# Optimization experiments

Hardware: AMD Instinct MI355X
Metric: run time of the kernel (lower is better)

## Reference

```python
import jax, jax.numpy as jnp
import numpy as np

E = 8          # number of routed experts
TOP_K = 2      # experts per token
D = 2048       # hidden size
DFF = 1408     # per-expert intermediate
DFF_S = 2816   # shared-expert intermediate (2 shared experts fused)
B, S = 2, 2048


def setup_inputs() -> dict:
    key = jax.random.key(0)
    ks = jax.random.split(key, 8)
    sc = 0.02
    return {
        "hidden_states": jax.random.normal(ks[0], (B, S, D), jnp.float32),
        "gate_weight": jax.random.normal(ks[1], (E, D), jnp.float32) * sc,
        "w_gate": jax.random.normal(ks[2], (E, DFF, D), jnp.float32) * sc,
        "w_up": jax.random.normal(ks[3], (E, DFF, D), jnp.float32) * sc,
        "w_down": jax.random.normal(ks[4], (E, D, DFF), jnp.float32) * sc,
        "w_shared_gate": jax.random.normal(ks[5], (DFF_S, D), jnp.float32) * sc,
        "w_shared_up": jax.random.normal(ks[6], (DFF_S, D), jnp.float32) * sc,
        "w_shared_down": jax.random.normal(ks[7], (D, DFF_S), jnp.float32) * sc,
    }


def reference(hidden_states, gate_weight, w_gate, w_up, w_down,
              w_shared_gate, w_shared_up, w_shared_down):
    orig_shape = hidden_states.shape
    x = hidden_states.reshape(-1, orig_shape[-1])      # [T, D]

    # --- router (computed under no_grad in the original) ---
    logits = x @ gate_weight.T                          # [T, E]
    scores = jax.nn.softmax(logits, axis=-1)
    topk_w, topk_idx = jax.lax.top_k(scores, TOP_K)     # [T, K]
    topk_w = topk_w / jnp.sum(topk_w, axis=-1, keepdims=True)
    topk_w = jax.lax.stop_gradient(topk_w)
    topk_idx = jax.lax.stop_gradient(topk_idx)

    # dense combine weights [T, E] (equivalent to the masked per-expert loop +
    # weighted sum over the top-k copies)
    combine = jnp.einsum('tk,tke->te', topk_w,
                         jax.nn.one_hot(topk_idx, E, dtype=x.dtype))

    # --- routed experts: SwiGLU MLP per expert, dense over E ---
    g = jnp.einsum('td,efd->etf', x, w_gate)            # [E, T, DFF]
    u = jnp.einsum('td,efd->etf', x, w_up)
    h = jax.nn.silu(g) * u
    expert_out = jnp.einsum('etf,edf->etd', h, w_down)  # [E, T, D]
    y = jnp.einsum('etd,te->td', expert_out, combine)   # [T, D]

    # --- shared experts on the identity ---
    sh = jax.nn.silu(x @ w_shared_gate.T) * (x @ w_shared_up.T)
    y = y + sh @ w_shared_down.T

    return y.reshape(orig_shape)
```

## Files before the change

kernel.cpp:

```cpp
#include <hip/hip_runtime.h>
#include <stdint.h>
#include <stdio.h>

#define T_TOK 4096
#define DMODEL 2048
#define NEXP 8
#define DFF 1408
#define DFFS 2816
#define NSLOT 8192

#define GU_GRID (16 * 22 + 39 * 11)
#define DN_GRID (16 * 8 + 39 * 8)
#define CONV_GU 1024
#define CONV_DN 512

typedef unsigned short u16;
typedef short s16x8 __attribute__((ext_vector_type(8)));
typedef unsigned short u16x4 __attribute__((ext_vector_type(4)));
typedef __bf16 bf16x8 __attribute__((ext_vector_type(8)));
typedef float f32x4 __attribute__((ext_vector_type(4)));

__device__ __forceinline__ u16 f2bf(float f) {
  uint32_t u = __builtin_bit_cast(uint32_t, f);
  u += 0x7fffu + ((u >> 16) & 1u);
  return (u16)(u >> 16);
}
__device__ __forceinline__ float bf2f(u16 h) {
  uint32_t u = ((uint32_t)h) << 16;
  return __builtin_bit_cast(float, u);
}

__device__ __forceinline__ void gl16(const u16* g, u16* l) {
  __builtin_amdgcn_global_load_lds((const __attribute__((address_space(1))) void*)g,
                                   (__attribute__((address_space(3))) void*)l,
                                   16, 0, 0);
}

#define BARRIER() asm volatile("s_barrier" ::: "memory")
#define SBAR()    __builtin_amdgcn_sched_barrier(0)

__device__ __forceinline__ void conv8(const float* __restrict__ s, u16* __restrict__ d,
                                      long k) {
  float4 a = ((const float4*)s)[2 * k];
  float4 b = ((const float4*)s)[2 * k + 1];
  s16x8 r;
  r[0] = (short)f2bf(a.x); r[1] = (short)f2bf(a.y);
  r[2] = (short)f2bf(a.z); r[3] = (short)f2bf(a.w);
  r[4] = (short)f2bf(b.x); r[5] = (short)f2bf(b.y);
  r[6] = (short)f2bf(b.z); r[7] = (short)f2bf(b.w);
  ((s16x8*)d)[k] = r;
}

__global__ void k_zero(int* __restrict__ counts) {
  if (threadIdx.x < NEXP) counts[threadIdx.x] = 0;
}

__global__ void k_router(const float* __restrict__ x, const float* __restrict__ gw,
                         u16* __restrict__ xb,
                         float* __restrict__ tkw, int* __restrict__ tki,
                         int* __restrict__ counts,
                         const float* __restrict__ wgF, u16* __restrict__ wbg,
                         const float* __restrict__ wuF, u16* __restrict__ wbu,
                         const float* __restrict__ wsgF, u16* __restrict__ wbsg,
                         const float* __restrict__ wsuF, u16* __restrict__ wbsu) {
  if (blockIdx.x >= T_TOK) {
    const long N1 = (long)NEXP * DFF * DMODEL / 8;
    const long NS = (long)DFFS * DMODEL / 8;
    const long total = 2 * N1 + 2 * NS;
    const long stride = (long)CONV_GU * 256;
    for (long i = (long)(blockIdx.x - T_TOK) * 256 + threadIdx.x; i < total; i += stride) {
      long k = i;
      if (k < N1)            conv8(wgF, wbg, k);
      else { k -= N1;
        if (k < N1)          conv8(wuF, wbu, k);
        else { k -= N1;
          if (k < NS)        conv8(wsgF, wbsg, k);
          else               conv8(wsuF, wbsu, k - NS);
        }
      }
    }
    return;
  }
  __shared__ double sm[NEXP];
  int t = blockIdx.x;
  int tid = threadIdx.x;
  int lane = tid & 63, wv = tid >> 6;
  const float4* xr = (const float4*)(x + (size_t)t * DMODEL);
  const float4* gr = (const float4*)gw;
  int e0 = wv * 2, e1 = e0 + 1;
  double a0 = 0.0, a1 = 0.0;
#pragma unroll
  for (int it = 0; it < DMODEL / 4 / 64; ++it) {
    int idx = it * 64 + lane;
    float4 xv = xr[idx];
    float4 g0 = gr[e0 * (DMODEL / 4) + idx];
    float4 g1 = gr[e1 * (DMODEL / 4) + idx];
    a0 += (double)xv.x * g0.x + (double)xv.y * g0.y +
          (double)xv.z * g0.z + (double)xv.w * g0.w;
    a1 += (double)xv.x * g1.x + (double)xv.y * g1.y +
          (double)xv.z * g1.z + (double)xv.w * g1.w;
    if (wv == 0) {
      u16x4 r = { f2bf(xv.x), f2bf(xv.y), f2bf(xv.z), f2bf(xv.w) };
      ((u16x4*)(xb + (size_t)t * DMODEL))[idx] = r;
    }
  }
#pragma unroll
  for (int off = 32; off; off >>= 1) {
    a0 += __shfl_down(a0, off, 64);
    a1 += __shfl_down(a1, off, 64);
  }
  if (lane == 0) { sm[e0] = a0; sm[e1] = a1; }
  __syncthreads();
  if (tid == 0) {
    double acc[NEXP];
#pragma unroll
    for (int e = 0; e < NEXP; ++e) acc[e] = sm[e];
    int i0 = 0; double v0 = acc[0];
    for (int e = 1; e < NEXP; ++e) if (acc[e] > v0) { v0 = acc[e]; i0 = e; }
    int i1 = -1; double v1 = -1e300;
    for (int e = 0; e < NEXP; ++e) if (e != i0 && acc[e] > v1) { v1 = acc[e]; i1 = e; }
    double r = exp(v1 - v0);
    float w0 = (float)(1.0 / (1.0 + r));
    float w1 = 1.0f - w0;
    tkw[2 * t] = w0; tkw[2 * t + 1] = w1;
    tki[2 * t] = i0; tki[2 * t + 1] = i1;
    atomicAdd(&counts[i0], 1);
    atomicAdd(&counts[i1], 1);
  }
}

__global__ void k_scan_sched(const int* __restrict__ counts, int* __restrict__ offs,
                             int* __restrict__ cursor, int* __restrict__ tblGU,
                             int* __restrict__ tblDN, int* __restrict__ nact) {
  if (threadIdx.x != 0 || blockIdx.x != 0) return;
  int s = 0;
  for (int e = 0; e < NEXP; ++e) { offs[e] = s; cursor[e] = s; s += counts[e]; }
  offs[NEXP] = s;
  int g = 0, d = 0;
  for (int m = 0; m < T_TOK / 256; ++m) {
    for (int nb = 0; nb < DFFS / 128; ++nb)
      tblGU[g++] = (int)(0x80000000u | (m << 12) | nb);
    for (int nb = 0; nb < DMODEL / 256; ++nb)
      tblDN[d++] = (int)(0x80000000u | (m << 12) | nb);
  }
  for (int e = 0; e < NEXP; ++e) {
    int mb = (counts[e] + 255) >> 8;
    for (int m = 0; m < mb; ++m) {
      for (int nb = 0; nb < DFF / 128; ++nb)
        tblGU[g++] = (e << 24) | (m << 12) | nb;
      for (int nb = 0; nb < DMODEL / 256; ++nb)
        tblDN[d++] = (e << 24) | (m << 12) | nb;
    }
  }
  nact[0] = g; nact[1] = d;
}

__global__ void k_assign(const int* __restrict__ tki, int* __restrict__ cursor,
                         int* __restrict__ pos, int* __restrict__ slot_tok) {
  int t = blockIdx.x * 256 + threadIdx.x;
  if (t >= T_TOK) return;
#pragma unroll
  for (int k = 0; k < 2; ++k) {
    int e = tki[2 * t + k];
    int p = atomicAdd(&cursor[e], 1);
    pos[2 * t + k] = p;
    slot_tok[p] = t;
  }
}

template <int PHASE>
__launch_bounds__(512, 2)
__global__ void k_gemm8(const int* __restrict__ tbl, const int* __restrict__ nact,
                        const u16* __restrict__ xb,
                        const u16* __restrict__ hr, const u16* __restrict__ hs,
                        const u16* __restrict__ wbg, const u16* __restrict__ wbu,
                        const u16* __restrict__ wbd,
                        const u16* __restrict__ wbsg, const u16* __restrict__ wbsu,
                        const u16* __restrict__ wbsd,
                        const float* __restrict__ wdF, const float* __restrict__ wsdF,
                        u16* __restrict__ wbdW, u16* __restrict__ wbsdW,
                        u16* __restrict__ P1r, u16* __restrict__ P1s,
                        u16* __restrict__ yr, float* __restrict__ out,
                        const int* __restrict__ offs, const int* __restrict__ counts,
                        const int* __restrict__ slot_tok) {
  __shared__ __attribute__((aligned(16))) u16 lds[2 * 32768];

  if constexpr (PHASE == 0) {
    if ((int)blockIdx.x >= GU_GRID) {
      const long N1 = (long)NEXP * DMODEL * DFF / 8;
      const long NS = (long)DMODEL * DFFS / 8;
      const long total = N1 + NS;
      const long stride = (long)CONV_DN * 512;
      for (long i = (long)(blockIdx.x - GU_GRID) * 512 + threadIdx.x; i < total;
           i += stride) {
        if (i < N1) conv8(wdF, wbdW, i);
        else        conv8(wsdF, wbsdW, i - N1);
      }
      return;
    }
  }
  if ((int)blockIdx.x >= nact[PHASE]) return;
  const int desc = tbl[blockIdx.x];
  const bool shrd = desc < 0;
  const int e = (desc >> 24) & 0xF;
  const int m0 = ((desc >> 12) & 0xFFF) * 256;
  const int n0 = (desc & 0xFFF) * (PHASE == 0 ? 128 : 256);

  const u16 *A, *Bg, *Bu;
  u16* C1;
  float* OF = nullptr;
  int base, cnt, HS, K;
  bool gather = false;
  if constexpr (PHASE == 0) {
    K = DMODEL;
    if (shrd) {
      A = xb; base = 0; cnt = T_TOK;
      Bg = wbsg; Bu = wbsu; C1 = P1s; HS = DFFS;
    } else {
      A = xb; gather = true; base = offs[e]; cnt = counts[e];
      size_t es = (size_t)e * DFF * DMODEL;
      Bg = wbg + es; Bu = wbu + es; C1 = P1r; HS = DFF;
    }
  } else {
    HS = DMODEL;
    if (shrd) {
      A = hs; base = 0; cnt = T_TOK; K = DFFS;
      Bg = Bu = wbsd; OF = out; C1 = nullptr;
    } else {
      A = hr; base = offs[e]; cnt = counts[e]; K = DFF;
      Bg = Bu = wbd + (size_t)e * DMODEL * DFF; C1 = yr;
    }
  }
  const int NT = K >> 6;

  int tid = threadIdx.x;
  int lane = tid & 63, wv = tid >> 6;
  int wm = wv >> 2, wn = wv & 3;
  int fr = lane & 15, fq = lane >> 4;

  int srow = tid >> 3;
  int sslot = (tid & 7) ^ (srow & 7);
  const u16* ap[4]; const u16* bp[4];
#pragma unroll
  for (int h = 0; h < 4; ++h) {
    int r = h * 64 + srow;
    int ra = m0 + r; ra = ra < cnt ? ra : cnt - 1;
    int ga = gather ? slot_tok[base + ra] : base + ra;
    ap[h] = A + (size_t)ga * K + sslot * 8;
    const u16* bb;
    if constexpr (PHASE == 0) {
      int wnr = r >> 6, s = r & 63;
      int col = n0 + wnr * 32 + (s & 31);
      bb = (s < 32 ? Bg : Bu) + (size_t)col * K;
    } else {
      bb = Bg + (size_t)(n0 + r) * K;
    }
    bp[h] = bb + sslot * 8;
  }

#define STG_A(h, bufi, kt) gl16(ap[h] + (size_t)(kt) * 64, \
                                lds + (bufi) * 32768 + (h) * 4096 + wv * 512)
#define STG_B(h, bufi, kt) gl16(bp[h] + (size_t)(kt) * 64, \
                                lds + (bufi) * 32768 + 16384 + (h) * 4096 + wv * 512)

  int sKs0 = ((0 + fq) ^ (fr & 7)) * 8;
  int sKs1 = ((4 + fq) ^ (fr & 7)) * 8;
  int aBase = wm * 8192 + fr * 64;
  int bBase = 16384 + (wn >> 1) * 8192 + ((wn & 1) * 64 + fr) * 64;

  f32x4 acc[8][4];
#pragma unroll
  for (int i = 0; i < 8; ++i)
#pragma unroll
    for (int j = 0; j < 4; ++j) acc[i][j] = (f32x4){0.f, 0.f, 0.f, 0.f};

  STG_A(0, 0, 0); STG_A(1, 0, 0); STG_A(2, 0, 0); STG_A(3, 0, 0);
  STG_B(0, 0, 0); STG_B(1, 0, 0); STG_B(2, 0, 0); STG_B(3, 0, 0);
  if (NT > 1) { STG_A(0, 1, 1); STG_A(1, 1, 1); STG_A(2, 1, 1); STG_A(3, 1, 1); }
  if (NT > 1) asm volatile("s_waitcnt vmcnt(4)" ::: "memory");
  else        asm volatile("s_waitcnt vmcnt(0)" ::: "memory");
  BARRIER();
  SBAR();

  bf16x8 rAa[4][2], rAb[4][2], rB01[2][2], rB23[2][2];
#pragma unroll
  for (int il = 0; il < 4; ++il) {
    rAa[il][0] = *(const bf16x8*)(lds + aBase + il * 1024 + sKs0);
    rAa[il][1] = *(const bf16x8*)(lds + aBase + il * 1024 + sKs1);
  }
#pragma unroll
  for (int jl = 0; jl < 2; ++jl) {
    rB01[jl][0] = *(const bf16x8*)(lds + bBase + jl * 1024 + sKs0);
    rB01[jl][1] = *(const bf16x8*)(lds + bBase + jl * 1024 + sKs1);
  }

  for (int t = 0; t < NT; ++t) {
    const int buf = t & 1, nbuf = buf ^ 1;
    const u16* lbuf = lds + buf * 32768;
    const u16* lbufN = lds + nbuf * 32768;
    const bool hn1 = (t + 1) < NT, hn2 = (t + 2) < NT;

#pragma unroll
    for (int jl = 0; jl < 2; ++jl) {
      rB23[jl][0] = *(const bf16x8*)(lbuf + bBase + (2 + jl) * 1024 + sKs0);
      rB23[jl][1] = *(const bf16x8*)(lbuf + bBase + (2 + jl) * 1024 + sKs1);
    }
    if (hn1) { STG_B(0, nbuf, t + 1); STG_B(1, nbuf, t + 1); }
    __builtin_amdgcn_s_setprio(1);
#pragma unroll
    for (int il = 0; il < 4; ++il)
#pragma unroll
      for (int jl = 0; jl < 2; ++jl) {
        acc[il][jl] = __builtin_amdgcn_mfma_f32_16x16x32_bf16(rAa[il][0], rB01[jl][0], acc[il][jl], 0, 0, 0);
        acc[il][jl] = __builtin_amdgcn_mfma_f32_16x16x32_bf16(rAa[il][1], rB01[jl][1], acc[il][jl], 0, 0, 0);
      }
    __builtin_amdgcn_s_setprio(0);

#pragma unroll
    for (int il = 0; il < 4; ++il) {
      rAb[il][0] = *(const bf16x8*)(lbuf + aBase + (4 + il) * 1024 + sKs0);
      rAb[il][1] = *(const bf16x8*)(lbuf + aBase + (4 + il) * 1024 + sKs1);
    }
    if (hn1) { STG_B(2, nbuf, t + 1); STG_B(3, nbuf, t + 1); }
    __builtin_amdgcn_s_setprio(1);
#pragma unroll
    for (int il = 0; il < 4; ++il)
#pragma unroll
      for (int jl = 0; jl < 2; ++jl) {
        acc[il][2 + jl] = __builtin_amdgcn_mfma_f32_16x16x32_bf16(rAa[il][0], rB23[jl][0], acc[il][2 + jl], 0, 0, 0);
        acc[il][2 + jl] = __builtin_amdgcn_mfma_f32_16x16x32_bf16(rAa[il][1], rB23[jl][1], acc[il][2 + jl], 0, 0, 0);
      }
    __builtin_amdgcn_s_setprio(0);

    asm volatile("s_waitcnt lgkmcnt(0)" ::: "memory");
    BARRIER();
    SBAR();
    if (hn2) { STG_A(0, buf, t + 2); STG_A(1, buf, t + 2); }
    __builtin_amdgcn_s_setprio(1);
#pragma unroll
    for (int il = 0; il < 4; ++il)
#pragma unroll
      for (int jl = 0; jl < 2; ++jl) {
        acc[4 + il][jl] = __builtin_amdgcn_mfma_f32_16x16x32_bf16(rAb[il][0], rB01[jl][0], acc[4 + il][jl], 0, 0, 0);
        acc[4 + il][jl] = __builtin_amdgcn_mfma_f32_16x16x32_bf16(rAb[il][1], rB01[jl][1], acc[4 + il][jl], 0, 0, 0);
      }
    __builtin_amdgcn_s_setprio(0);

    if (hn1) {
      if (hn2) asm volatile("s_waitcnt vmcnt(2)" ::: "memory");
      else     asm volatile("s_waitcnt vmcnt(0)" ::: "memory");
      BARRIER();
      SBAR();
      if (hn2) { STG_A(2, buf, t + 2); STG_A(3, buf, t + 2); }
#pragma unroll
      for (int il = 0; il < 4; ++il) {
        rAa[il][0] = *(const bf16x8*)(lbufN + aBase + il * 1024 + sKs0);
        rAa[il][1] = *(const bf16x8*)(lbufN + aBase + il * 1024 + sKs1);
      }
#pragma unroll
      for (int jl = 0; jl < 2; ++jl) {
        rB01[jl][0] = *(const bf16x8*)(lbufN + bBase + jl * 1024 + sKs0);
        rB01[jl][1] = *(const bf16x8*)(lbufN + bBase + jl * 1024 + sKs1);
      }
    }
    __builtin_amdgcn_s_setprio(1);
#pragma unroll
    for (int il = 0; il < 4; ++il)
#pragma unroll
      for (int jl = 0; jl < 2; ++jl) {
        acc[4 + il][2 + jl] = __builtin_amdgcn_mfma_f32_16x16x32_bf16(rAb[il][0], rB23[jl][0], acc[4 + il][2 + jl], 0, 0, 0);
        acc[4 + il][2 + jl] = __builtin_amdgcn_mfma_f32_16x16x32_bf16(rAb[il][1], rB23[jl][1], acc[4 + il][2 + jl], 0, 0, 0);
      }
    __builtin_amdgcn_s_setprio(0);
  }
#undef STG_A
#undef STG_B

#pragma unroll
  for (int i = 0; i < 8; ++i) {
    int row_t = wm * 128 + i * 16 + fq * 4;
#pragma unroll
    for (int r = 0; r < 4; ++r) {
      int m = m0 + row_t + r;
      if (m >= cnt) continue;
      size_t rowoff = (size_t)(base + m) * (size_t)HS;
      if constexpr (PHASE == 0) {
#pragma unroll
        for (int jl = 0; jl < 2; ++jl) {
          float g = acc[i][jl][r];
          float u = acc[i][2 + jl][r];
          float hval = (g / (1.f + __expf(-g))) * u;
          C1[rowoff + (n0 + wn * 32 + jl * 16 + fr)] = f2bf(hval);
        }
      } else {
#pragma unroll
        for (int j = 0; j < 4; ++j) {
          int col_t = n0 + wn * 64 + j * 16 + fr;
          float v = acc[i][j][r];
          if (shrd) OF[rowoff + col_t] = v;
          else      C1[rowoff + col_t] = f2bf(v);
        }
      }
    }
  }
}

__global__ void k_combine(float* __restrict__ y, const u16* __restrict__ yr,
                          const float* __restrict__ tkw, const int* __restrict__ pos) {
  int t = blockIdx.x;
  int i = threadIdx.x;
  float w0 = tkw[2 * t], w1 = tkw[2 * t + 1];
  size_t p0 = (size_t)pos[2 * t] * DMODEL, p1 = (size_t)pos[2 * t + 1] * DMODEL;
  int d0 = i * 8;
  s16x8 a = *(const s16x8*)(yr + p0 + d0);
  s16x8 b = *(const s16x8*)(yr + p1 + d0);
  float* yo = y + (size_t)t * DMODEL + d0;
#pragma unroll
  for (int j = 0; j < 8; ++j)
    yo[j] += w0 * bf2f((u16)a[j]) + w1 * bf2f((u16)b[j]);
}

extern "C" void kernel_launch(void* const* d_in, const int* in_sizes, int n_in,
                              void* d_out, int out_size, void* d_ws, size_t ws_size,
                              hipStream_t stream) {
  const float* x   = (const float*)d_in[0];
  const float* gw  = (const float*)d_in[1];
  const float* wg  = (const float*)d_in[2];
  const float* wu  = (const float*)d_in[3];
  const float* wd  = (const float*)d_in[4];
  const float* wsg = (const float*)d_in[5];
  const float* wsu = (const float*)d_in[6];
  const float* wsd = (const float*)d_in[7];
  float* out = (float*)d_out;

  char* ws = (char*)d_ws;
  size_t o = 0;
  auto alloc = [&](size_t bytes) -> void* {
    void* p = ws + o;
    o += (bytes + 255) & ~(size_t)255;
    return p;
  };
  u16* xb   = (u16*)alloc((size_t)T_TOK * DMODEL * 2);
  u16* wbg  = (u16*)alloc((size_t)NEXP * DFF * DMODEL * 2);
  u16* wbu  = (u16*)alloc((size_t)NEXP * DFF * DMODEL * 2);
  u16* wbd  = (u16*)alloc((size_t)NEXP * DMODEL * DFF * 2);
  u16* wbsg = (u16*)alloc((size_t)DFFS * DMODEL * 2);
  u16* wbsu = (u16*)alloc((size_t)DFFS * DMODEL * 2);
  u16* wbsd = (u16*)alloc((size_t)DMODEL * DFFS * 2);
  u16* P1r  = (u16*)alloc((size_t)NSLOT * DFF * 2);
  u16* P1s  = (u16*)alloc((size_t)T_TOK * DFFS * 2);
  u16* yr   = (u16*)alloc((size_t)NSLOT * DMODEL * 2);
  float* tkw = (float*)alloc((size_t)T_TOK * 2 * 4);
  int* tki   = (int*)alloc((size_t)T_TOK * 2 * 4);
  int* pos   = (int*)alloc((size_t)T_TOK * 2 * 4);
  int* slot_tok = (int*)alloc((size_t)NSLOT * 4);
  int* counts   = (int*)alloc(64);
  int* offs     = (int*)alloc(64);
  int* cursor   = (int*)alloc(64);
  int* tblGU    = (int*)alloc(GU_GRID * 4);
  int* tblDN    = (int*)alloc(DN_GRID * 4);
  int* nact     = (int*)alloc(64);
  if (o > ws_size) {
    fprintf(stderr, "kernel_launch: ws too small: need %zu have %zu\n", o, ws_size);
    return;
  }

  k_zero<<<1, 64, 0, stream>>>(counts);
  k_router<<<T_TOK + CONV_GU, 256, 0, stream>>>(x, gw, xb, tkw, tki, counts,
                                                wg, wbg, wu, wbu, wsg, wbsg, wsu, wbsu);
  k_scan_sched<<<1, 64, 0, stream>>>(counts, offs, cursor, tblGU, tblDN, nact);
  k_assign<<<(T_TOK + 255) / 256, 256, 0, stream>>>(tki, cursor, pos, slot_tok);

  k_gemm8<0><<<GU_GRID + CONV_DN, 512, 0, stream>>>(
      tblGU, nact, xb, nullptr, nullptr,
      wbg, wbu, wbd, wbsg, wbsu, wbsd,
      wd, wsd, wbd, wbsd,
      P1r, P1s, yr, out, offs, counts, slot_tok);

  k_gemm8<1><<<DN_GRID, 512, 0, stream>>>(
      tblDN, nact, xb, P1r, P1s,
      wbg, wbu, wbd, wbsg, wbsu, wbsd,
      nullptr, nullptr, nullptr, nullptr,
      P1r, P1s, yr, out, offs, counts, slot_tok);

  k_combine<<<T_TOK, 256, 0, stream>>>(out, yr, tkw, pos);
}
```

Measured before the change: 534.9 us.

## Move down-proj weight conversion from gate/up GEMM into router kernel

The fp32-to-bf16 conversion of the routed and shared down-projection weights now runs in the router kernel's extra blocks, next to the gate/up weight conversion, instead of in extra blocks of the phase-0 GEMM launch. The converter block count grows so all six weight tensors are handled in one pass. The GEMM phase-0 launch drops its conversion tail and runs only GEMM tiles, so conversion traffic no longer competes with GEMM compute. In exchange the router kernel carries more memory-bound work before the GEMMs can start, and it no longer overlaps with compute.

```diff
diff --git a/kernel.cpp b/kernel.cpp
--- a/kernel.cpp
+++ b/kernel.cpp
@@ -11,8 +11,7 @@
 
 #define GU_GRID (16 * 22 + 39 * 11)
 #define DN_GRID (16 * 8 + 39 * 8)
-#define CONV_GU 1024
-#define CONV_DN 512
+#define CONV_ALL 1536
 
 typedef unsigned short u16;
 typedef short s16x8 __attribute__((ext_vector_type(8)));
@@ -62,12 +61,14 @@
                          const float* __restrict__ wgF, u16* __restrict__ wbg,
                          const float* __restrict__ wuF, u16* __restrict__ wbu,
                          const float* __restrict__ wsgF, u16* __restrict__ wbsg,
-                         const float* __restrict__ wsuF, u16* __restrict__ wbsu) {
+                         const float* __restrict__ wsuF, u16* __restrict__ wbsu,
+                         const float* __restrict__ wdF, u16* __restrict__ wbd,
+                         const float* __restrict__ wsdF, u16* __restrict__ wbsd) {
   if (blockIdx.x >= T_TOK) {
     const long N1 = (long)NEXP * DFF * DMODEL / 8;
     const long NS = (long)DFFS * DMODEL / 8;
-    const long total = 2 * N1 + 2 * NS;
-    const long stride = (long)CONV_GU * 256;
+    const long total = 3 * N1 + 3 * NS;
+    const long stride = (long)CONV_ALL * 256;
     for (long i = (long)(blockIdx.x - T_TOK) * 256 + threadIdx.x; i < total; i += stride) {
       long k = i;
       if (k < N1)            conv8(wgF, wbg, k);
@@ -75,7 +76,13 @@
         if (k < N1)          conv8(wuF, wbu, k);
         else { k -= N1;
           if (k < NS)        conv8(wsgF, wbsg, k);
-          else               conv8(wsuF, wbsu, k - NS);
+          else { k -= NS;
+            if (k < NS)      conv8(wsuF, wbsu, k);
+            else { k -= NS;
+              if (k < N1)    conv8(wdF, wbd, k);
+              else           conv8(wsdF, wbsd, k - N1);
+            }
+          }
         }
       }
     }
@@ -177,28 +184,12 @@
                         const u16* __restrict__ wbd,
                         const u16* __restrict__ wbsg, const u16* __restrict__ wbsu,
                         const u16* __restrict__ wbsd,
-                        const float* __restrict__ wdF, const float* __restrict__ wsdF,
-                        u16* __restrict__ wbdW, u16* __restrict__ wbsdW,
                         u16* __restrict__ P1r, u16* __restrict__ P1s,
                         u16* __restrict__ yr, float* __restrict__ out,
                         const int* __restrict__ offs, const int* __restrict__ counts,
                         const int* __restrict__ slot_tok) {
   __shared__ __attribute__((aligned(16))) u16 lds[2 * 32768];
 
-  if constexpr (PHASE == 0) {
-    if ((int)blockIdx.x >= GU_GRID) {
-      const long N1 = (long)NEXP * DMODEL * DFF / 8;
-      const long NS = (long)DMODEL * DFFS / 8;
-      const long total = N1 + NS;
-      const long stride = (long)CONV_DN * 512;
-      for (long i = (long)(blockIdx.x - GU_GRID) * 512 + threadIdx.x; i < total;
-           i += stride) {
-        if (i < N1) conv8(wdF, wbdW, i);
-        else        conv8(wsdF, wbsdW, i - N1);
-      }
-      return;
-    }
-  }
   if ((int)blockIdx.x >= nact[PHASE]) return;
   const int desc = tbl[blockIdx.x];
   const bool shrd = desc < 0;
@@ -466,21 +457,20 @@
   }
 
   k_zero<<<1, 64, 0, stream>>>(counts);
-  k_router<<<T_TOK + CONV_GU, 256, 0, stream>>>(x, gw, xb, tkw, tki, counts,
-                                                wg, wbg, wu, wbu, wsg, wbsg, wsu, wbsu);
+  k_router<<<T_TOK + CONV_ALL, 256, 0, stream>>>(x, gw, xb, tkw, tki, counts,
+                                                 wg, wbg, wu, wbu, wsg, wbsg, wsu, wbsu,
+                                                 wd, wbd, wsd, wbsd);
   k_scan_sched<<<1, 64, 0, stream>>>(counts, offs, cursor, tblGU, tblDN, nact);
   k_assign<<<(T_TOK + 255) / 256, 256, 0, stream>>>(tki, cursor, pos, slot_tok);
 
-  k_gemm8<0><<<GU_GRID + CONV_DN, 512, 0, stream>>>(
+  k_gemm8<0><<<GU_GRID, 512, 0, stream>>>(
       tblGU, nact, xb, nullptr, nullptr,
       wbg, wbu, wbd, wbsg, wbsu, wbsd,
-      wd, wsd, wbd, wbsd,
       P1r, P1s, yr, out, offs, counts, slot_tok);
 
   k_gemm8<1><<<DN_GRID, 512, 0, stream>>>(
       tblDN, nact, xb, P1r, P1s,
       wbg, wbu, wbd, wbsg, wbsu, wbsd,
-      nullptr, nullptr, nullptr, nullptr,
       P1r, P1s, yr, out, offs, counts, slot_tok);
 
   k_combine<<<T_TOK, 256, 0, stream>>>(out, yr, tkw, pos);
```

After: 552.0 us. 3.2% more time.
